# Optimization experiments

Measured on AMD Instinct MI355X. Metric: run time of the kernel, lower is better.

The kernel has to match this reference:

```python
import jax, jax.numpy as jnp
import numpy as np

B, C, H, W = 16, 256, 64, 64
NH, HD, NM = 4, 32, 4  # heads, head_dim, memory tokens
HID = NH * HD


def rms_norm(x, g):
    # F.normalize(x, dim=1) * sqrt(C) * g  (channel dim = 1)
    norm = jnp.maximum(jnp.linalg.norm(x, axis=1, keepdims=True), 1e-12)
    return x / norm * (x.shape[1] ** 0.5) * g


def setup_inputs() -> dict:
    key = jax.random.key(0)
    ks = jax.random.split(key, 5)
    return {
        "x": jax.random.normal(ks[0], (B, C, H, W), jnp.float32),
        "g_in": jnp.ones((1, C, 1, 1), jnp.float32),
        "mem_kv": jax.random.normal(ks[1], (2, NH, HD, NM), jnp.float32),
        "w_qkv": jax.random.normal(ks[2], (HID * 3, C), jnp.float32) * (C ** -0.5),
        "w_out": jax.random.normal(ks[3], (C, HID), jnp.float32) * (HID ** -0.5),
        "b_out": jnp.zeros((C,), jnp.float32),
        "g_out": jnp.ones((1, C, 1, 1), jnp.float32),
    }


def reference(x, g_in, mem_kv, w_qkv, w_out, b_out, g_out):
    b, c, h, w = x.shape
    n = h * w
    scale = HD ** -0.5

    xn = rms_norm(x, g_in)
    # 1x1 conv as matmul over channel dim: [B, 3*HID, H, W]
    qkv = jnp.einsum('oc,bchw->bohw', w_qkv, xn)
    q, k, v = jnp.split(qkv, 3, axis=1)
    # b (h d) x y -> b h d n
    q = q.reshape(b, NH, HD, n)
    k = k.reshape(b, NH, HD, n)
    v = v.reshape(b, NH, HD, n)

    # prepend memory key/value tokens: [b, h, d, NM + n]
    mk = jnp.broadcast_to(mem_kv[0], (b, NH, HD, NM))
    mv = jnp.broadcast_to(mem_kv[1], (b, NH, HD, NM))
    k = jnp.concatenate([mk, k], axis=-1)
    v = jnp.concatenate([mv, v], axis=-1)

    q = jax.nn.softmax(q, axis=-2) * scale  # softmax over head_dim
    k = jax.nn.softmax(k, axis=-1)          # softmax over tokens

    context = jnp.einsum('bhdn,bhen->bhde', k, v)  # [b, h, d, e]
    out = jnp.einsum('bhde,bhdn->bhen', context, q)  # [b, h, e, n]
    out = out.reshape(b, HID, h, w)

    out = jnp.einsum('oc,bchw->bohw', w_out, out) + b_out[None, :, None, None]
    return rms_norm(out, g_out)
```

## Files before the change

kernel.cpp:

```cpp
#include <hip/hip_runtime.h>
#include <math.h>

typedef unsigned short u16;
typedef unsigned int u32;

#define NBATCH 16
#define NCH    256
#define NPIX   4096
#define NHEAD  4
#define HDIM   32
#define NMEM   4
#define HID    128
#define OC3    384
#define SCALE_Q 0.17677669529663687f

typedef __bf16 bf16x8 __attribute__((ext_vector_type(8)));
typedef float  f32x4  __attribute__((ext_vector_type(4)));

__device__ __forceinline__ u16 bfb(float f){
  union { __bf16 h; u16 u; } x; x.h = (__bf16)f; return x.u;
}
__device__ __forceinline__ u32 pkbf2(float a, float b){
  union { __bf16 h[2]; u32 u; } x; x.h[0] = (__bf16)a; x.h[1] = (__bf16)b; return x.u;
}
__device__ __forceinline__ void gload_lds16(const void* gp, void* lp){
  __builtin_amdgcn_global_load_lds(
      (const __attribute__((address_space(1))) unsigned int*)gp,
      (__attribute__((address_space(3))) unsigned int*)lp, 16, 0, 0);
}

__global__ __launch_bounds__(256) void k_pack(const float* __restrict__ wqkv,
                                              const float* __restrict__ gin,
                                              const float* __restrict__ wout,
                                              const float* __restrict__ memkv,
                                              u16* __restrict__ wqb,
                                              u16* __restrict__ wob,
                                              float* __restrict__ ctxmem,
                                              float* __restrict__ zmem)
{
  int i = blockIdx.x*256 + threadIdx.x;
  if (i < OC3*NCH){ int c = i & 255; wqb[i] = bfb(wqkv[i]*gin[c]); }
  else if (i < OC3*NCH + NCH*HID){ int j = i - OC3*NCH; wob[j] = bfb(wout[j]); }
  else {
    int j = i - (OC3*NCH + NCH*HID);
    if (j < 4096){
      int h = j>>10, d = (j>>5)&31, e = j&31;
      float s = 0.f;
      #pragma unroll
      for (int m=0;m<4;m++)
        s += __expf(memkv[(h*HDIM+d)*NMEM + m]) * memkv[512 + (h*HDIM+e)*NMEM + m];
      ctxmem[j] = s;
    } else if (j < 4224){
      int k = j - 4096; int h = k>>5, d = k&31;
      float s = 0.f;
      #pragma unroll
      for (int m=0;m<4;m++) s += __expf(memkv[(h*HDIM+d)*NMEM + m]);
      zmem[k] = s;
    }
  }
}

__global__ __launch_bounds__(512, 4) void k_qkvx(const float* __restrict__ x,
                                                 const u16* __restrict__ wqb,
                                                 u16* __restrict__ qt,
                                                 float* __restrict__ ctxa,
                                                 float* __restrict__ za)
{
  __shared__ __align__(16) char smem[52480];
  float (*Xs)[64]   = (float(*)[64])smem;
  u16*   Bx         = (u16*)(smem + 16384);
  float (*ssqp)[64] = (float(*)[64])(smem + 50176);
  float* rl         = (float*)(smem + 52224);
  u16*   Ek         = (u16*)smem;
  u16*   Vv         = (u16*)(smem + 18432);
  float (*psx)[64]  = (float(*)[64])(smem + 36864);

  const int t = threadIdx.x, w = t>>6, lane = t&63;
  const int n0 = blockIdx.x*64, b = blockIdx.y;
  const int qw = lane>>4, rr = lane&15;

  {
    float ssq = 0.f;
    for (int s=0;s<4;++s){
      asm volatile("s_waitcnt lgkmcnt(0)" ::: "memory");
      const float* gp = x + ((size_t)b*NCH + s*64 + w*8 + (lane>>4))*NPIX + n0 + (lane&15)*4;
      gload_lds16(gp,                    &Xs[w*8 + 0][0]);
      gload_lds16(gp + (size_t)4*NPIX,   &Xs[w*8 + 4][0]);
      asm volatile("s_waitcnt vmcnt(0)" ::: "memory");
      u32 pk[4];
      #pragma unroll
      for (int q=0;q<4;q++){
        float v0 = Xs[w*8 + 2*q    ][lane];
        float v1 = Xs[w*8 + 2*q + 1][lane];
        ssq += v0*v0 + v1*v1;
        pk[q] = pkbf2(v0, v1);
      }
      *(int4*)&Bx[lane*264 + s*64 + w*8] = make_int4((int)pk[0],(int)pk[1],(int)pk[2],(int)pk[3]);
    }
    ssqp[w][lane] = ssq;
  }
  __syncthreads();
  if (t < 64){
    float s = 0.f;
    #pragma unroll
    for (int g=0;g<8;g++) s += ssqp[g][t];
    rl[t] = 16.0f / fmaxf(sqrtf(s), 1e-12f);
  }

  f32x4 acc[3][4];
  #pragma unroll
  for (int p=0;p<3;p++)
    #pragma unroll
    for (int nf=0;nf<4;nf++) acc[p][nf] = (f32x4){0.f,0.f,0.f,0.f};

  const u16* aw = wqb + (size_t)(w*16 + rr)*NCH + qw*8;
  bf16x8 caf0 = *(const bf16x8*)(aw);
  bf16x8 caf1 = *(const bf16x8*)(aw + 128*NCH);
  bf16x8 caf2 = *(const bf16x8*)(aw + 256*NCH);
  #pragma unroll
  for (int c0=0; c0<NCH; c0+=32){
    bf16x8 bfr[4];
    #pragma unroll
    for (int nf=0;nf<4;nf++)
      bfr[nf] = *(const bf16x8*)&Bx[(nf*16+rr)*264 + c0 + qw*8];
    bf16x8 naf0 = caf0, naf1 = caf1, naf2 = caf2;
    if (c0 < NCH-32){
      naf0 = *(const bf16x8*)(aw + c0+32);
      naf1 = *(const bf16x8*)(aw + 128*NCH + c0+32);
      naf2 = *(const bf16x8*)(aw + 256*NCH + c0+32);
    }
    #pragma unroll
    for (int nf=0;nf<4;nf++){
      acc[0][nf] = __builtin_amdgcn_mfma_f32_16x16x32_bf16(caf0, bfr[nf], acc[0][nf], 0, 0, 0);
      acc[1][nf] = __builtin_amdgcn_mfma_f32_16x16x32_bf16(bfr[nf], caf1, acc[1][nf], 0, 0, 0);
      acc[2][nf] = __builtin_amdgcn_mfma_f32_16x16x32_bf16(bfr[nf], caf2, acc[2][nf], 0, 0, 0);
    }
    caf0 = naf0; caf1 = naf1; caf2 = naf2;
  }

  __syncthreads();

  float zk = 0.f;
  #pragma unroll
  for (int nf=0;nf<4;nf++){
    const float4 rv4 = *(const float4*)&rl[nf*16 + qw*4];
    float e0 = __expf(acc[1][nf][0]*rv4.x);
    float e1 = __expf(acc[1][nf][1]*rv4.y);
    float e2 = __expf(acc[1][nf][2]*rv4.z);
    float e3 = __expf(acc[1][nf][3]*rv4.w);
    zk += e0+e1+e2+e3;
    *(int2*)&Ek[(w*16+rr)*72 + nf*16 + qw*4] =
        make_int2((int)pkbf2(e0,e1), (int)pkbf2(e2,e3));
    float v0 = acc[2][nf][0]*rv4.x, v1 = acc[2][nf][1]*rv4.y;
    float v2 = acc[2][nf][2]*rv4.z, v3 = acc[2][nf][3]*rv4.w;
    *(int2*)&Vv[(w*16+rr)*72 + nf*16 + qw*4] =
        make_int2((int)pkbf2(v0,v1), (int)pkbf2(v2,v3));
  }
  zk += __shfl_xor(zk, 16, 64);
  zk += __shfl_xor(zk, 32, 64);

  float qv[4][4], pm[4], ps[4];
  #pragma unroll
  for (int nf=0;nf<4;nf++){
    float rv = rl[nf*16 + rr];
    float m = -1e30f;
    #pragma unroll
    for (int r=0;r<4;r++){ qv[nf][r] = acc[0][nf][r]*rv; m = fmaxf(m, qv[nf][r]); }
    m = fmaxf(m, __shfl_xor(m, 16, 64));
    m = fmaxf(m, __shfl_xor(m, 32, 64));
    float s = 0.f;
    #pragma unroll
    for (int r=0;r<4;r++){ qv[nf][r] = __expf(qv[nf][r]-m); s += qv[nf][r]; }
    s += __shfl_xor(s, 16, 64);
    s += __shfl_xor(s, 32, 64);
    pm[nf] = m; ps[nf] = s;
  }
  if (lane < 16){
    #pragma unroll
    for (int nf=0;nf<4;nf++){ ssqp[w][nf*16+lane] = pm[nf]; psx[w][nf*16+lane] = ps[nf]; }
  }
  __syncthreads();
  {
    const int pw = w^1;
    u16* qbase = qt + ((size_t)b*NPIX + n0)*HID + w*16 + qw*4;
    #pragma unroll
    for (int nf=0;nf<4;nf++){
      float om = ssqp[pw][nf*16+rr], os = psx[pw][nf*16+rr];
      float M = fmaxf(pm[nf], om);
      float S = ps[nf]*__expf(pm[nf]-M) + os*__expf(om-M);
      float f = __expf(pm[nf]-M) * SCALE_Q / S;
      u32 lo = pkbf2(qv[nf][0]*f, qv[nf][1]*f);
      u32 hi = pkbf2(qv[nf][2]*f, qv[nf][3]*f);
      *(int2*)(qbase + (size_t)(nf*16+rr)*HID) = make_int2((int)lo,(int)hi);
    }
  }

  {
    const int h = w>>1, eh = w&1;
    f32x4 pacc[2] = {(f32x4){0.f,0.f,0.f,0.f},(f32x4){0.f,0.f,0.f,0.f}};
    #pragma unroll
    for (int ks=0; ks<2; ks++){
      bf16x8 bv = *(const bf16x8*)&Vv[(h*32+eh*16+rr)*72 + ks*32 + qw*8];
      #pragma unroll
      for (int i=0;i<2;i++){
        bf16x8 ae = *(const bf16x8*)&Ek[(h*32+i*16+rr)*72 + ks*32 + qw*8];
        pacc[i] = __builtin_amdgcn_mfma_f32_16x16x32_bf16(ae, bv, pacc[i], 0, 0, 0);
      }
    }
    float* pb = ctxa + (size_t)b*4096 + h*1024;
    #pragma unroll
    for (int i=0;i<2;i++)
      #pragma unroll
      for (int reg=0;reg<4;reg++)
        atomicAdd(&pb[(i*16+qw*4+reg)*32 + eh*16 + rr], pacc[i][reg]);
    if (qw==0) atomicAdd(&za[b*128 + w*16 + rr], zk);
  }
}

__global__ __launch_bounds__(256) void k_fout(const u16* __restrict__ qt,
                                              const float* __restrict__ ctxa,
                                              const float* __restrict__ za,
                                              const float* __restrict__ ctxmem,
                                              const float* __restrict__ zmem,
                                              const u16* __restrict__ wob,
                                              const float* __restrict__ bout,
                                              const float* __restrict__ gout,
                                              float* __restrict__ out)
{
  __shared__ u16 Cb[4*32*40];
  __shared__ u16 Ao[64*136];
  __shared__ float ssql[4][64];
  const int t = threadIdx.x, w = t>>6, lane = t&63;
  const int n0 = blockIdx.x*64, b = blockIdx.y;
  const int qw = lane>>4, rr = lane&15;

  {
    const int d = (t>>3)&31, e0 = (t&7)*4;
    #pragma unroll
    for (int h=0;h<4;h++){
      float4 a = *(const float4*)(ctxa + (size_t)b*4096 + h*1024 + d*32 + e0);
      float4 m = *(const float4*)(ctxmem + h*1024 + d*32 + e0);
      float rinv = 1.0f / (za[b*128 + h*32 + d] + zmem[h*32 + d]);
      Cb[(h*32+e0+0)*40 + d] = bfb((a.x+m.x)*rinv);
      Cb[(h*32+e0+1)*40 + d] = bfb((a.y+m.y)*rinv);
      Cb[(h*32+e0+2)*40 + d] = bfb((a.z+m.z)*rinv);
      Cb[(h*32+e0+3)*40 + d] = bfb((a.w+m.w)*rinv);
    }
  }
  __syncthreads();

  f32x4 pv[4][2];
  const u16* qp = qt + ((size_t)b*NPIX + n0 + w*16 + rr)*HID;
  #pragma unroll
  for (int h=0;h<4;h++){
    bf16x8 bq = *(const bf16x8*)(qp + h*32 + qw*8);
    #pragma unroll
    for (int ef=0;ef<2;ef++){
      bf16x8 af = *(const bf16x8*)&Cb[(h*32 + ef*16 + rr)*40 + qw*8];
      f32x4 z = (f32x4){0.f,0.f,0.f,0.f};
      pv[h][ef] = __builtin_amdgcn_mfma_f32_16x16x32_bf16(af, bq, z, 0, 0, 0);
    }
  }
  #pragma unroll
  for (int h=0;h<4;h++)
    #pragma unroll
    for (int ef=0;ef<2;ef++){
      u32 lohi0 = pkbf2(pv[h][ef][0], pv[h][ef][1]);
      u32 lohi1 = pkbf2(pv[h][ef][2], pv[h][ef][3]);
      *(int2*)&Ao[(w*16+rr)*136 + h*32 + ef*16 + qw*4] = make_int2((int)lohi0,(int)lohi1);
    }
  __syncthreads();

  f32x4 acc[4][4];
  #pragma unroll
  for (int i=0;i<4;i++)
    #pragma unroll
    for (int j=0;j<4;j++) acc[i][j] = (f32x4){0.f,0.f,0.f,0.f};
  #pragma unroll
  for (int k0=0; k0<HID; k0+=32){
    bf16x8 af[4], bfr[4];
    #pragma unroll
    for (int mf=0;mf<4;mf++)
      af[mf] = *(const bf16x8*)&wob[(size_t)(w*64 + mf*16 + rr)*HID + k0 + qw*8];
    #pragma unroll
    for (int nf=0;nf<4;nf++)
      bfr[nf] = *(const bf16x8*)&Ao[(nf*16+rr)*136 + k0 + qw*8];
    #pragma unroll
    for (int mf=0;mf<4;mf++)
      #pragma unroll
      for (int nf=0;nf<4;nf++)
        acc[mf][nf] = __builtin_amdgcn_mfma_f32_16x16x32_bf16(af[mf], bfr[nf], acc[mf][nf], 0, 0, 0);
  }
  float pssq[4] = {0.f,0.f,0.f,0.f};
  #pragma unroll
  for (int mf=0;mf<4;mf++)
    #pragma unroll
    for (int reg=0;reg<4;reg++){
      int c = w*64 + mf*16 + qw*4 + reg;
      float bb = bout[c];
      #pragma unroll
      for (int nf=0;nf<4;nf++){
        float v = acc[mf][nf][reg] + bb;
        acc[mf][nf][reg] = v;
        pssq[nf] += v*v;
      }
    }
  #pragma unroll
  for (int nf=0;nf<4;nf++){
    pssq[nf] += __shfl_xor(pssq[nf], 16, 64);
    pssq[nf] += __shfl_xor(pssq[nf], 32, 64);
  }
  if (qw==0){
    #pragma unroll
    for (int nf=0;nf<4;nf++) ssql[w][nf*16+rr] = pssq[nf];
  }
  __syncthreads();
  float rv[4];
  #pragma unroll
  for (int nf=0;nf<4;nf++){
    int col = nf*16 + rr;
    float sm = ssql[0][col]+ssql[1][col]+ssql[2][col]+ssql[3][col];
    rv[nf] = 16.0f / fmaxf(sqrtf(sm), 1e-12f);
  }
  #pragma unroll
  for (int mf=0;mf<4;mf++)
    #pragma unroll
    for (int reg=0;reg<4;reg++){
      int c = w*64 + mf*16 + qw*4 + reg;
      float g = gout[c];
      float* po = out + ((size_t)(b*NCH + c))*NPIX + n0;
      #pragma unroll
      for (int nf=0;nf<4;nf++)
        po[nf*16 + rr] = acc[mf][nf][reg]*rv[nf]*g;
    }
}

extern "C" void kernel_launch(void* const* d_in, const int* in_sizes, int n_in,
                              void* d_out, int out_size, void* d_ws, size_t ws_size,
                              hipStream_t stream)
{
  const float* x     = (const float*)d_in[0];
  const float* gin   = (const float*)d_in[1];
  const float* memkv = (const float*)d_in[2];
  const float* wqkv  = (const float*)d_in[3];
  const float* wout  = (const float*)d_in[4];
  const float* bout  = (const float*)d_in[5];
  const float* gout  = (const float*)d_in[6];
  float* out = (float*)d_out;

  char* ws = (char*)d_ws;
  u16*    qt     = (u16*)   (ws);
  float*  ctxa   = (float*) (ws + 16777216);
  float*  za     = (float*) (ws + 17039360);
  float*  ctxmem = (float*) (ws + 17047552);
  float*  zmem   = (float*) (ws + 17063936);
  u16*    wqb    = (u16*)   (ws + 17064448);
  u16*    wob    = (u16*)   (ws + 17261056);

  hipMemsetAsync(ws + 16777216, 0, 270336, stream);

  hipLaunchKernelGGL(k_pack, dim3(529),   dim3(256), 0, stream,
                     wqkv, gin, wout, memkv, wqb, wob, ctxmem, zmem);
  hipLaunchKernelGGL(k_qkvx, dim3(64,16), dim3(512), 0, stream, x, wqb, qt, ctxa, za);
  hipLaunchKernelGGL(k_fout, dim3(64,16), dim3(256), 0, stream,
                     qt, ctxa, za, ctxmem, zmem, wob, bout, gout, out);
}
```

Baseline: 175.4 us.

## Fold context into output projection per batch and replace atomics with partial buffers

Each k_qkvx block now writes its per-tile context and normalizer partials to a dedicated slice, which replaces the global float atomics and the memset. A new k_w2 kernel sums those partials, normalizes the context, and multiplies it into w_out to form a per-batch 256x128 combined weight W2 = w_out·ctx^T. k_fout then runs a single GEMM of q against W2, dropping the context-apply MFMA stage and its LDS staging, and stores output as float4. The cost is an extra launch, about 17MB of partial buffer traffic, a serial 64-step reduction in k_w2 spread over only 64 blocks, and one more bf16 rounding of the combined weight.

```diff
diff --git a/kernel.cpp b/kernel.cpp
--- a/kernel.cpp
+++ b/kernel.cpp
@@ -63,8 +63,7 @@
 __global__ __launch_bounds__(512, 4) void k_qkvx(const float* __restrict__ x,
                                                  const u16* __restrict__ wqb,
                                                  u16* __restrict__ qt,
-                                                 float* __restrict__ ctxa,
-                                                 float* __restrict__ za)
+                                                 float* __restrict__ ctxp2)
 {
   __shared__ __align__(16) char smem[52480];
   float (*Xs)[64]   = (float(*)[64])smem;
@@ -207,132 +206,174 @@
         pacc[i] = __builtin_amdgcn_mfma_f32_16x16x32_bf16(ae, bv, pacc[i], 0, 0, 0);
       }
     }
-    float* pb = ctxa + (size_t)b*4096 + h*1024;
+    float* pb = ctxp2 + ((size_t)((b*64 + blockIdx.x)*4 + h))*1088;
     #pragma unroll
     for (int i=0;i<2;i++)
       #pragma unroll
       for (int reg=0;reg<4;reg++)
-        atomicAdd(&pb[(i*16+qw*4+reg)*32 + eh*16 + rr], pacc[i][reg]);
-    if (qw==0) atomicAdd(&za[b*128 + w*16 + rr], zk);
-  }
+        pb[(i*16+qw*4+reg)*32 + eh*16 + rr] = pacc[i][reg];
+    if (qw==0) pb[1024 + (w&1)*16 + rr] = zk;
+  }
+}
+
+__global__ __launch_bounds__(256) void k_w2(const float* __restrict__ ctxp2,
+                                            const float* __restrict__ ctxmem,
+                                            const float* __restrict__ zmem,
+                                            const u16* __restrict__ wob,
+                                            u16* __restrict__ w2b)
+{
+  __shared__ u16 Ct[32][40];
+  __shared__ float zps[8][32];
+  __shared__ float rinv[32];
+  const int bh = blockIdx.x, b = bh>>2, h = bh&3;
+  const int t = threadIdx.x, w = t>>6, lane = t&63;
+  const int qw = lane>>4, rr = lane&15;
+  const int d = t>>3, e0 = (t&7)*4;
+
+  const float* base = ctxp2 + ((size_t)(b*64)*4 + h)*1088;
+  float4 ps = make_float4(0.f,0.f,0.f,0.f);
+  for (int s=0;s<64;s++){
+    float4 v = *(const float4*)(base + (size_t)s*4*1088 + d*32 + e0);
+    ps.x+=v.x; ps.y+=v.y; ps.z+=v.z; ps.w+=v.w;
+  }
+  {
+    int dz = t&31, sg = t>>5;
+    float zp = 0.f;
+    for (int s=sg*8; s<sg*8+8; s++) zp += base[(size_t)s*4*1088 + 1024 + dz];
+    zps[sg][dz] = zp;
+  }
+  __syncthreads();
+  if (t < 32){
+    float z = zmem[h*32 + t];
+    #pragma unroll
+    for (int g=0;g<8;g++) z += zps[g][t];
+    rinv[t] = 1.0f / z;
+  }
+  __syncthreads();
+  {
+    float ri = rinv[d];
+    const float* cm = ctxmem + h*1024 + d*32 + e0;
+    Ct[d][e0+0] = bfb((ps.x + cm[0])*ri);
+    Ct[d][e0+1] = bfb((ps.y + cm[1])*ri);
+    Ct[d][e0+2] = bfb((ps.z + cm[2])*ri);
+    Ct[d][e0+3] = bfb((ps.w + cm[3])*ri);
+  }
+  __syncthreads();
+  f32x4 pacc[4][2];
+  #pragma unroll
+  for (int mf=0;mf<4;mf++)
+    #pragma unroll
+    for (int nd=0;nd<2;nd++) pacc[mf][nd] = (f32x4){0.f,0.f,0.f,0.f};
+  bf16x8 be[2];
+  be[0] = *(const bf16x8*)&Ct[rr][qw*8];
+  be[1] = *(const bf16x8*)&Ct[16+rr][qw*8];
+  #pragma unroll
+  for (int mf=0;mf<4;mf++){
+    bf16x8 af = *(const bf16x8*)&wob[(size_t)(w*64+mf*16+rr)*HID + h*32 + qw*8];
+    #pragma unroll
+    for (int nd=0;nd<2;nd++)
+      pacc[mf][nd] = __builtin_amdgcn_mfma_f32_16x16x32_bf16(af, be[nd], pacc[mf][nd], 0, 0, 0);
+  }
+  #pragma unroll
+  for (int mf=0;mf<4;mf++)
+    #pragma unroll
+    for (int nd=0;nd<2;nd++)
+      #pragma unroll
+      for (int reg=0;reg<4;reg++)
+        w2b[((size_t)b*NCH + w*64+mf*16+qw*4+reg)*HID + h*32 + nd*16 + rr] =
+            bfb(pacc[mf][nd][reg]);
 }
 
 __global__ __launch_bounds__(256) void k_fout(const u16* __restrict__ qt,
-                                              const float* __restrict__ ctxa,
-                                              const float* __restrict__ za,
-                                              const float* __restrict__ ctxmem,
-                                              const float* __restrict__ zmem,
-                                              const u16* __restrict__ wob,
+                                              const u16* __restrict__ w2b,
                                               const float* __restrict__ bout,
                                               const float* __restrict__ gout,
                                               float* __restrict__ out)
 {
-  __shared__ u16 Cb[4*32*40];
-  __shared__ u16 Ao[64*136];
   __shared__ float ssql[4][64];
   const int t = threadIdx.x, w = t>>6, lane = t&63;
   const int n0 = blockIdx.x*64, b = blockIdx.y;
   const int qw = lane>>4, rr = lane&15;
 
-  {
-    const int d = (t>>3)&31, e0 = (t&7)*4;
-    #pragma unroll
-    for (int h=0;h<4;h++){
-      float4 a = *(const float4*)(ctxa + (size_t)b*4096 + h*1024 + d*32 + e0);
-      float4 m = *(const float4*)(ctxmem + h*1024 + d*32 + e0);
-      float rinv = 1.0f / (za[b*128 + h*32 + d] + zmem[h*32 + d]);
-      Cb[(h*32+e0+0)*40 + d] = bfb((a.x+m.x)*rinv);
-      Cb[(h*32+e0+1)*40 + d] = bfb((a.y+m.y)*rinv);
-      Cb[(h*32+e0+2)*40 + d] = bfb((a.z+m.z)*rinv);
-      Cb[(h*32+e0+3)*40 + d] = bfb((a.w+m.w)*rinv);
-    }
-  }
-  __syncthreads();
-
-  f32x4 pv[4][2];
-  const u16* qp = qt + ((size_t)b*NPIX + n0 + w*16 + rr)*HID;
-  #pragma unroll
-  for (int h=0;h<4;h++){
-    bf16x8 bq = *(const bf16x8*)(qp + h*32 + qw*8);
-    #pragma unroll
-    for (int ef=0;ef<2;ef++){
-      bf16x8 af = *(const bf16x8*)&Cb[(h*32 + ef*16 + rr)*40 + qw*8];
-      f32x4 z = (f32x4){0.f,0.f,0.f,0.f};
-      pv[h][ef] = __builtin_amdgcn_mfma_f32_16x16x32_bf16(af, bq, z, 0, 0, 0);
-    }
-  }
-  #pragma unroll
-  for (int h=0;h<4;h++)
-    #pragma unroll
-    for (int ef=0;ef<2;ef++){
-      u32 lohi0 = pkbf2(pv[h][ef][0], pv[h][ef][1]);
-      u32 lohi1 = pkbf2(pv[h][ef][2], pv[h][ef][3]);
-      *(int2*)&Ao[(w*16+rr)*136 + h*32 + ef*16 + qw*4] = make_int2((int)lohi0,(int)lohi1);
-    }
-  __syncthreads();
-
   f32x4 acc[4][4];
   #pragma unroll
   for (int i=0;i<4;i++)
     #pragma unroll
     for (int j=0;j<4;j++) acc[i][j] = (f32x4){0.f,0.f,0.f,0.f};
-  #pragma unroll
-  for (int k0=0; k0<HID; k0+=32){
-    bf16x8 af[4], bfr[4];
+
+  const u16* qbase = qt + ((size_t)b*NPIX + n0)*HID;
+  const u16* wbase = w2b + (size_t)b*NCH*HID;
+  #pragma unroll
+  for (int k0=0;k0<HID;k0+=32){
+    bf16x8 bq[4], aw[4];
+    #pragma unroll
+    for (int nf=0;nf<4;nf++)
+      bq[nf] = *(const bf16x8*)(qbase + (size_t)(nf*16+rr)*HID + k0 + qw*8);
     #pragma unroll
     for (int mf=0;mf<4;mf++)
-      af[mf] = *(const bf16x8*)&wob[(size_t)(w*64 + mf*16 + rr)*HID + k0 + qw*8];
+      aw[mf] = *(const bf16x8*)(wbase + (size_t)(w*64+mf*16+rr)*HID + k0 + qw*8);
+    #pragma unroll
+    for (int mf=0;mf<4;mf++)
+      #pragma unroll
+      for (int nf=0;nf<4;nf++)
+        acc[mf][nf] = __builtin_amdgcn_mfma_f32_16x16x32_bf16(bq[nf], aw[mf], acc[mf][nf], 0, 0, 0);
+  }
+  float psq[4][4] = {{0.f}};
+  #pragma unroll
+  for (int mf=0;mf<4;mf++){
+    float bb = bout[w*64+mf*16+rr];
     #pragma unroll
     for (int nf=0;nf<4;nf++)
-      bfr[nf] = *(const bf16x8*)&Ao[(nf*16+rr)*136 + k0 + qw*8];
-    #pragma unroll
-    for (int mf=0;mf<4;mf++)
-      #pragma unroll
-      for (int nf=0;nf<4;nf++)
-        acc[mf][nf] = __builtin_amdgcn_mfma_f32_16x16x32_bf16(af[mf], bfr[nf], acc[mf][nf], 0, 0, 0);
-  }
-  float pssq[4] = {0.f,0.f,0.f,0.f};
-  #pragma unroll
-  for (int mf=0;mf<4;mf++)
-    #pragma unroll
-    for (int reg=0;reg<4;reg++){
-      int c = w*64 + mf*16 + qw*4 + reg;
-      float bb = bout[c];
-      #pragma unroll
-      for (int nf=0;nf<4;nf++){
+      #pragma unroll
+      for (int reg=0;reg<4;reg++){
         float v = acc[mf][nf][reg] + bb;
         acc[mf][nf][reg] = v;
-        pssq[nf] += v*v;
+        psq[nf][reg] += v*v;
       }
-    }
+  }
+  #pragma unroll
+  for (int nf=0;nf<4;nf++)
+    #pragma unroll
+    for (int reg=0;reg<4;reg++){
+      psq[nf][reg] += __shfl_xor(psq[nf][reg], 1, 64);
+      psq[nf][reg] += __shfl_xor(psq[nf][reg], 2, 64);
+      psq[nf][reg] += __shfl_xor(psq[nf][reg], 4, 64);
+      psq[nf][reg] += __shfl_xor(psq[nf][reg], 8, 64);
+    }
+  if (rr==0){
+    #pragma unroll
+    for (int nf=0;nf<4;nf++)
+      #pragma unroll
+      for (int reg=0;reg<4;reg++)
+        ssql[w][nf*16+qw*4+reg] = psq[nf][reg];
+  }
+  __syncthreads();
+  float4 rv4[4];
   #pragma unroll
   for (int nf=0;nf<4;nf++){
-    pssq[nf] += __shfl_xor(pssq[nf], 16, 64);
-    pssq[nf] += __shfl_xor(pssq[nf], 32, 64);
-  }
-  if (qw==0){
-    #pragma unroll
-    for (int nf=0;nf<4;nf++) ssql[w][nf*16+rr] = pssq[nf];
-  }
-  __syncthreads();
-  float rv[4];
-  #pragma unroll
-  for (int nf=0;nf<4;nf++){
-    int col = nf*16 + rr;
-    float sm = ssql[0][col]+ssql[1][col]+ssql[2][col]+ssql[3][col];
-    rv[nf] = 16.0f / fmaxf(sqrtf(sm), 1e-12f);
-  }
-  #pragma unroll
-  for (int mf=0;mf<4;mf++)
-    #pragma unroll
-    for (int reg=0;reg<4;reg++){
-      int c = w*64 + mf*16 + qw*4 + reg;
-      float g = gout[c];
-      float* po = out + ((size_t)(b*NCH + c))*NPIX + n0;
-      #pragma unroll
-      for (int nf=0;nf<4;nf++)
-        po[nf*16 + rr] = acc[mf][nf][reg]*rv[nf]*g;
-    }
+    float4 s0 = *(const float4*)&ssql[0][nf*16+qw*4];
+    float4 s1 = *(const float4*)&ssql[1][nf*16+qw*4];
+    float4 s2 = *(const float4*)&ssql[2][nf*16+qw*4];
+    float4 s3 = *(const float4*)&ssql[3][nf*16+qw*4];
+    rv4[nf].x = 16.0f / fmaxf(sqrtf(s0.x+s1.x+s2.x+s3.x), 1e-12f);
+    rv4[nf].y = 16.0f / fmaxf(sqrtf(s0.y+s1.y+s2.y+s3.y), 1e-12f);
+    rv4[nf].z = 16.0f / fmaxf(sqrtf(s0.z+s1.z+s2.z+s3.z), 1e-12f);
+    rv4[nf].w = 16.0f / fmaxf(sqrtf(s0.w+s1.w+s2.w+s3.w), 1e-12f);
+  }
+  #pragma unroll
+  for (int mf=0;mf<4;mf++){
+    float g = gout[w*64+mf*16+rr];
+    float* po = out + ((size_t)(b*NCH + w*64+mf*16+rr))*NPIX + n0;
+    #pragma unroll
+    for (int nf=0;nf<4;nf++){
+      float4 o4;
+      o4.x = acc[mf][nf][0]*rv4[nf].x*g;
+      o4.y = acc[mf][nf][1]*rv4[nf].y*g;
+      o4.z = acc[mf][nf][2]*rv4[nf].z*g;
+      o4.w = acc[mf][nf][3]*rv4[nf].w*g;
+      *(float4*)(po + nf*16 + qw*4) = o4;
+    }
+  }
 }
 
 extern "C" void kernel_launch(void* const* d_in, const int* in_sizes, int n_in,
@@ -350,18 +391,18 @@
 
   char* ws = (char*)d_ws;
   u16*    qt     = (u16*)   (ws);
-  float*  ctxa   = (float*) (ws + 16777216);
-  float*  za     = (float*) (ws + 17039360);
-  float*  ctxmem = (float*) (ws + 17047552);
-  float*  zmem   = (float*) (ws + 17063936);
-  u16*    wqb    = (u16*)   (ws + 17064448);
-  u16*    wob    = (u16*)   (ws + 17261056);
-
-  hipMemsetAsync(ws + 16777216, 0, 270336, stream);
+  float*  ctxp2  = (float*) (ws + 16777216);
+  u16*    w2b    = (u16*)   (ws + 34603008);
+  float*  ctxmem = (float*) (ws + 35651584);
+  float*  zmem   = (float*) (ws + 35667968);
+  u16*    wqb    = (u16*)   (ws + 35668480);
+  u16*    wob    = (u16*)   (ws + 35865088);
 
   hipLaunchKernelGGL(k_pack, dim3(529),   dim3(256), 0, stream,
                      wqkv, gin, wout, memkv, wqb, wob, ctxmem, zmem);
-  hipLaunchKernelGGL(k_qkvx, dim3(64,16), dim3(512), 0, stream, x, wqb, qt, ctxa, za);
+  hipLaunchKernelGGL(k_qkvx, dim3(64,16), dim3(512), 0, stream, x, wqb, qt, ctxp2);
+  hipLaunchKernelGGL(k_w2,   dim3(64),    dim3(256), 0, stream,
+                     ctxp2, ctxmem, zmem, wob, w2b);
   hipLaunchKernelGGL(k_fout, dim3(64,16), dim3(256), 0, stream,
-                     qt, ctxa, za, ctxmem, zmem, wob, bout, gout, out);
-}
+                     qt, w2b, bout, gout, out);
+}
```

Result: no change. 178.8 us (+1.9%).

## Replace global atomics for context accumulation with partial buffers and reduction kernel

Applied to the files above, without the earlier changes.

Each k_qkvx block now writes its per-head context and normalizer partials to a private slot in a new partial buffer instead of issuing atomicAdds to shared accumulators. A new k_red kernel sums 16 partials per group and then atomically adds the four group results into the final context and z arrays. The aim is to cut contention from 64 blocks per batch hitting the same addresses. In exchange it costs about 17 MB of extra workspace traffic and one more kernel launch.

```diff
diff --git a/kernel.cpp b/kernel.cpp
--- a/kernel.cpp
+++ b/kernel.cpp
@@ -63,8 +63,7 @@
 __global__ __launch_bounds__(512, 4) void k_qkvx(const float* __restrict__ x,
                                                  const u16* __restrict__ wqb,
                                                  u16* __restrict__ qt,
-                                                 float* __restrict__ ctxa,
-                                                 float* __restrict__ za)
+                                                 float* __restrict__ ctxp2)
 {
   __shared__ __align__(16) char smem[52480];
   float (*Xs)[64]   = (float(*)[64])smem;
@@ -207,13 +206,39 @@
         pacc[i] = __builtin_amdgcn_mfma_f32_16x16x32_bf16(ae, bv, pacc[i], 0, 0, 0);
       }
     }
-    float* pb = ctxa + (size_t)b*4096 + h*1024;
+    float* pb = ctxp2 + ((size_t)((b*64 + blockIdx.x)*4 + h))*1088;
     #pragma unroll
     for (int i=0;i<2;i++)
       #pragma unroll
       for (int reg=0;reg<4;reg++)
-        atomicAdd(&pb[(i*16+qw*4+reg)*32 + eh*16 + rr], pacc[i][reg]);
-    if (qw==0) atomicAdd(&za[b*128 + w*16 + rr], zk);
+        pb[(i*16+qw*4+reg)*32 + eh*16 + rr] = pacc[i][reg];
+    if (qw==0) pb[1024 + (w&1)*16 + rr] = zk;
+  }
+}
+
+__global__ __launch_bounds__(256) void k_red(const float* __restrict__ ctxp2,
+                                             float* __restrict__ ctxa,
+                                             float* __restrict__ za)
+{
+  const int r = blockIdx.x;
+  const int b = r>>4, h = (r>>2)&3, g = r&3;
+  const int t = threadIdx.x;
+  const int d = t>>3, e0 = (t&7)*4;
+  const float* base = ctxp2 + ((size_t)((b*64 + g*16)*4) + h)*1088;
+  float4 sum = make_float4(0.f,0.f,0.f,0.f);
+  #pragma unroll
+  for (int s=0;s<16;s++){
+    float4 v = *(const float4*)(base + (size_t)s*4*1088 + d*32 + e0);
+    sum.x+=v.x; sum.y+=v.y; sum.z+=v.z; sum.w+=v.w;
+  }
+  float* pa = ctxa + (size_t)b*4096 + h*1024 + d*32 + e0;
+  atomicAdd(pa+0, sum.x); atomicAdd(pa+1, sum.y);
+  atomicAdd(pa+2, sum.z); atomicAdd(pa+3, sum.w);
+  if (t < 32){
+    float zs = 0.f;
+    #pragma unroll
+    for (int s=0;s<16;s++) zs += base[(size_t)s*4*1088 + 1024 + t];
+    atomicAdd(&za[b*128 + h*32 + t], zs);
   }
 }
 
@@ -350,18 +375,20 @@
 
   char* ws = (char*)d_ws;
   u16*    qt     = (u16*)   (ws);
-  float*  ctxa   = (float*) (ws + 16777216);
-  float*  za     = (float*) (ws + 17039360);
-  float*  ctxmem = (float*) (ws + 17047552);
-  float*  zmem   = (float*) (ws + 17063936);
-  u16*    wqb    = (u16*)   (ws + 17064448);
-  u16*    wob    = (u16*)   (ws + 17261056);
-
-  hipMemsetAsync(ws + 16777216, 0, 270336, stream);
+  float*  ctxp2  = (float*) (ws + 16777216);
+  float*  ctxa   = (float*) (ws + 34603008);
+  float*  za     = (float*) (ws + 34865152);
+  float*  ctxmem = (float*) (ws + 34873344);
+  float*  zmem   = (float*) (ws + 34889728);
+  u16*    wqb    = (u16*)   (ws + 34890240);
+  u16*    wob    = (u16*)   (ws + 35086848);
+
+  hipMemsetAsync(ws + 34603008, 0, 270336, stream);
 
   hipLaunchKernelGGL(k_pack, dim3(529),   dim3(256), 0, stream,
                      wqkv, gin, wout, memkv, wqb, wob, ctxmem, zmem);
-  hipLaunchKernelGGL(k_qkvx, dim3(64,16), dim3(512), 0, stream, x, wqb, qt, ctxa, za);
+  hipLaunchKernelGGL(k_qkvx, dim3(64,16), dim3(512), 0, stream, x, wqb, qt, ctxp2);
+  hipLaunchKernelGGL(k_red,  dim3(256),   dim3(256), 0, stream, ctxp2, ctxa, za);
   hipLaunchKernelGGL(k_fout, dim3(64,16), dim3(256), 0, stream,
                      qt, ctxa, za, ctxmem, zmem, wob, bout, gout, out);
 }
```

After: 172.9 us. No clear change (-1.5%).
